# Optimization experiments

Measured on AMD Instinct MI355X. Metric: run time of the kernel, lower is better.

## Reference

```python
import jax, jax.numpy as jnp
import numpy as np
from jax import lax

B, T = 1024, 1000
EPS = 1e-3  # keras BatchNormalization default epsilon
ALPHA = 0.2  # tf.nn.leaky_relu default alpha


def setup_inputs() -> dict:
    key = jax.random.key(0)
    ks = jax.random.split(key, 40)
    f32 = jnp.float32
    n = lambda k, s, sc=0.1: jax.random.normal(k, s, dtype=f32) * sc
    inp = {"x": jax.random.normal(ks[0], (B, 2, T, 1), dtype=f32)}
    # main conv stack (HWIO kernels)
    inp["c1k"] = n(ks[1], (1, 5, 1, 10));  inp["c1b"] = n(ks[2], (10,), 0.01)
    inp["c2k"] = n(ks[3], (1, 5, 10, 10)); inp["c2b"] = n(ks[4], (10,), 0.01)
    inp["c3k"] = n(ks[5], (1, 5, 10, 10)); inp["c3b"] = n(ks[6], (10,), 0.01)
    inp["c4k"] = n(ks[7], (2, 1, 10, 20)); inp["c4b"] = n(ks[8], (20,), 0.01)
    # batchnorm (inference) params
    for i, k0 in zip((1, 2, 3), (9, 13, 17)):
        inp[f"g{i}"]  = 1.0 + n(ks[k0], (10,), 0.05)
        inp[f"be{i}"] = n(ks[k0 + 1], (10,), 0.05)
        inp[f"m{i}"]  = n(ks[k0 + 2], (10,), 0.05)
        inp[f"v{i}"]  = 1.0 + jax.random.uniform(ks[k0 + 3], (10,), dtype=f32) * 0.1
    # dense head: flatten of [B,1,T-12,20]
    inp["dns_w"] = n(ks[21], ((T - 12) * 20, 1), 0.02)
    inp["dns_b"] = jnp.zeros((1,), f32)
    # MHRSSA blocks: 10 heads of Conv2D(2,(2,1)) stacked -> K [10,2,Cin,2], b [10,2];
    # depthwise (1,5) over 10 channels -> dw [5,10], db [10]
    inp["a1K"] = n(ks[22], (10, 2, 1, 2));  inp["a1b"] = n(ks[23], (10, 2), 0.01)
    inp["a1dw"] = n(ks[24], (5, 10));       inp["a1db"] = n(ks[25], (10,), 0.01)
    inp["a2K"] = n(ks[26], (10, 2, 10, 2)); inp["a2b"] = n(ks[27], (10, 2), 0.01)
    inp["a2dw"] = n(ks[28], (5, 10));       inp["a2db"] = n(ks[29], (10,), 0.01)
    inp["a3K"] = n(ks[30], (10, 2, 10, 2)); inp["a3b"] = n(ks[31], (10, 2), 0.01)
    inp["a3dw"] = n(ks[32], (5, 10));       inp["a3db"] = n(ks[33], (10,), 0.01)
    return inp


def conv2d(x, k, b):
    return lax.conv_general_dilated(x, k, (1, 1), 'VALID',
                                    dimension_numbers=('NHWC', 'HWIO', 'NHWC')) + b


def bn_inf(x, g, be, m, v):
    return (x - m) * (g * lax.rsqrt(v + EPS)) + be


def lrelu(x):
    return jnp.where(x >= 0, x, ALPHA * x)


def mhrssa(x, K, b, dw, db):
    # x: [B,2,T,C]; K: [10,2,C,2] (10 heads of a (2,1)-valid conv) -> [B,10,T,2]
    m = jnp.einsum('bhtc,ihco->bito', x, K) + b[None, :, None, :]
    a = jnp.transpose(m, (0, 3, 2, 1))  # [B,2,T,10]
    Tt = a.shape[2]
    # depthwise (1,5) valid conv over time, per-channel taps dw[w,i]
    y = sum(a[:, :, w:w + Tt - 4, :] * dw[w] for w in range(5)) + db
    return jax.nn.softmax(y, axis=-1)


def reference(x, c1k, c1b, g1, be1, m1, v1, c2k, c2b, g2, be2, m2, v2,
              c3k, c3b, g3, be3, m3, v3, c4k, c4b, dns_w, dns_b,
              a1K, a1b, a1dw, a1db, a2K, a2b, a2dw, a2db, a3K, a3b, a3dw, a3db):
    att1 = mhrssa(x, a1K, a1b, a1dw, a1db)
    h = lrelu(bn_inf(conv2d(x, c1k, c1b), g1, be1, m1, v1)) * att1
    att2 = mhrssa(h, a2K, a2b, a2dw, a2db)
    h = lrelu(bn_inf(conv2d(h, c2k, c2b), g2, be2, m2, v2)) * att2
    att3 = mhrssa(h, a3K, a3b, a3dw, a3db)
    h = lrelu(bn_inf(conv2d(h, c3k, c3b), g3, be3, m3, v3)) * att3
    h = lrelu(conv2d(h, c4k, c4b))          # [B,1,T-12,20]
    h = h.reshape(h.shape[0], -1)
    return h @ dns_w + dns_b                # RGS mode: raw scalar output
```

## Files before the change

### kernel.cpp

```cpp
#include <hip/hip_runtime.h>

#define REP10(X) X(0) X(1) X(2) X(3) X(4) X(5) X(6) X(7) X(8) X(9)
#define REP5(X)  X(0) X(1) X(2) X(3) X(4)

typedef __attribute__((ext_vector_type(2))) float v2;

#define SMMP 136

__device__ __forceinline__ void fold_stage(
    float* dst, const float* g, const float* be, const float* mn,
    const float* vr, const float* cb, const float* adw, const float* adb,
    const float* aK, const float* ab, int CIN)
{
  const int tid = threadIdx.x;
  if (tid < 10) {
    const float sc = g[tid] * rsqrtf(vr[tid] + 1e-3f);
    dst[tid]      = sc;
    dst[10 + tid] = (cb[tid] - mn[tid]) * sc + be[tid];
    dst[70 + tid] = adb[tid] * 1.44269504088896340736f;
  }
  if (tid >= 10 && tid < 60)
    dst[10 + tid] = adw[tid - 10] * 1.44269504088896340736f;
  if (tid < 20)
    dst[80 + tid] = ab[(tid % 10) * 2 + tid / 10];
  const int n = 2 * CIN * 2 * 10;
  for (int idx = tid; idx < n; idx += 64) {
    const int i  = idx % 10;
    const int r  = idx / 10;
    const int o  = r % 2;
    const int r2 = r / 2;
    const int ci = r2 % CIN;
    const int h  = r2 / CIN;
    dst[100 + idx] = aK[((i * 2 + h) * CIN + ci) * 2 + o];
  }
}

__global__ void prep_kernel(
    const float* g1, const float* be1, const float* m1, const float* v1,
    const float* cb1, const float* a1dw, const float* a1db,
    const float* a1K, const float* a1b,
    const float* g2, const float* be2, const float* m2, const float* v2_,
    const float* cb2, const float* a2dw, const float* a2db,
    const float* a2K, const float* a2b,
    const float* g3, const float* be3, const float* m3, const float* v3,
    const float* cb3, const float* a3dw, const float* a3db,
    const float* a3K, const float* a3b,
    float* consts)
{
  fold_stage(consts,        g1, be1, m1, v1,  cb1, a1dw, a1db, a1K, a1b, 1);
  fold_stage(consts + 512,  g2, be2, m2, v2_, cb2, a2dw, a2db, a2K, a2b, 10);
  fold_stage(consts + 1024, g3, be3, m3, v3,  cb3, a3dw, a3db, a3K, a3b, 10);
}

__global__ void transpose_dnsw(const float* __restrict__ dnsw,
                               float* __restrict__ dnswT)
{
  const int cc = blockIdx.x;
  for (int t = threadIdx.x; t < 988; t += 256)
    dnswT[cc * 988 + t] = dnsw[t * 20 + cc];
}

template <int CIN>
__global__ __launch_bounds__(128) void stage_kernel(
    const float* __restrict__ in, float* __restrict__ outp, int Tout,
    const float* __restrict__ ck, const float* __restrict__ cst)
{
  __shared__ float smm[5 * SMMP * 2];
  const int tid = threadIdx.x;
  const int o   = blockIdx.y;
  const int t0  = blockIdx.x * 128;
  const int Tin = Tout + 4;
  const float* __restrict__ inb = in + (size_t)blockIdx.z * (CIN * 2000);

  const float* __restrict__ scale  = cst;
  const float* __restrict__ shift2 = cst + 10;
  const float* __restrict__ adw2   = cst + 20;
  const float* __restrict__ adb2   = cst + 70;
  const float* __restrict__ abp    = cst + 80;
  const float* __restrict__ aKp    = cst + 100;

  for (int lt = tid; lt < 132; lt += 128) {
    const int t = t0 + lt;
    if (t < Tin) {
#define DECLM(p) v2 mp##p = *reinterpret_cast<const v2*>(abp + o * 10 + 2 * p);
      REP5(DECLM)
#undef DECLM
#pragma unroll
      for (int h = 0; h < 2; ++h)
#pragma unroll
        for (int ci = 0; ci < CIN; ++ci) {
          const float xin = inb[(ci * 2 + h) * 1000 + t];
          const v2 xs = {xin, xin};
          const float* kb = aKp + ((h * CIN + ci) * 2 + o) * 10;
#define FMAM(p) mp##p = __builtin_elementwise_fma(                             \
              xs, *reinterpret_cast<const v2*>(kb + 2 * p), mp##p);
          REP5(FMAM)
#undef FMAM
        }
#define STM(p) *reinterpret_cast<v2*>(&smm[(p * SMMP + lt) * 2]) = mp##p;
      REP5(STM)
#undef STM
    }
  }
  __syncthreads();

  const int tt = t0 + tid;
  if (tt >= Tout) return;

#define DECLY(p) v2 yp##p = *reinterpret_cast<const v2*>(adb2 + 2 * p);
  REP5(DECLY)
#undef DECLY
#pragma unroll
  for (int w = 0; w < 5; ++w) {
    const float* aw = adw2 + w * 10;
#define FMAY(p) { const v2 sv =                                                \
        *reinterpret_cast<const v2*>(&smm[(p * SMMP + tid + w) * 2]);          \
      yp##p = __builtin_elementwise_fma(                                       \
          sv, *reinterpret_cast<const v2*>(aw + 2 * p), yp##p); }
    REP5(FMAY)
#undef FMAY
  }

#define DECLA(p) v2 ap##p = {0.f, 0.f};
  REP5(DECLA)
#undef DECLA
  const float* __restrict__ cinb = inb + o * 1000 + tt;
#pragma unroll
  for (int w = 0; w < 5; ++w)
#pragma unroll
    for (int ci = 0; ci < CIN; ++ci) {
      const float xin = cinb[ci * 2000 + w];
      const v2 xs = {xin, xin};
      const float* kb = ck + (w * CIN + ci) * 10;
#define FMAC(p) ap##p = __builtin_elementwise_fma(                             \
          xs, *reinterpret_cast<const v2*>(kb + 2 * p), ap##p);
      REP5(FMAC)
#undef FMAC
    }

  const float y0 = yp0.x, y1 = yp0.y, y2 = yp1.x, y3 = yp1.y, y4 = yp2.x,
              y5 = yp2.y, y6 = yp3.x, y7 = yp3.y, y8 = yp4.x, y9 = yp4.y;
  float mx = y0;
  mx = fmaxf(mx, y1); mx = fmaxf(mx, y2); mx = fmaxf(mx, y3);
  mx = fmaxf(mx, y4); mx = fmaxf(mx, y5); mx = fmaxf(mx, y6);
  mx = fmaxf(mx, y7); mx = fmaxf(mx, y8); mx = fmaxf(mx, y9);
#define DECLE(i) const float e##i = exp2f(y##i - mx);
  REP10(DECLE)
#undef DECLE
  const float sm  = e0 + e1 + e2 + e3 + e4 + e5 + e6 + e7 + e8 + e9;
  const float inv = __builtin_amdgcn_rcpf(sm);

  const float a0 = ap0.x, a1 = ap0.y, a2 = ap1.x, a3 = ap1.y, a4 = ap2.x,
              a5 = ap2.y, a6 = ap3.x, a7 = ap3.y, a8 = ap4.x, a9 = ap4.y;
  float* __restrict__ ob = outp + (size_t)blockIdx.z * 20000 + o * 1000 + tt;
#define STO(i) { float bv = a##i * scale[i] + shift2[i];                       \
    bv = fmaxf(bv, 0.2f * bv);                                                 \
    ob[i * 2000] = bv * e##i * inv; }
  REP10(STO)
#undef STO
}

__global__ __launch_bounds__(256) void final_kernel(
    const float* __restrict__ h3, const float* __restrict__ c4k,
    const float* __restrict__ c4b, const float* __restrict__ dnswT,
    const float* __restrict__ dnsb, float* __restrict__ outp, int b0)
{
  __shared__ float red[4];
  const int tid = threadIdx.x;
  const float* __restrict__ hb = h3 + (size_t)blockIdx.x * 20000;
  float partial = 0.f;
#pragma unroll 1
  for (int t = 2 * tid; t < 988; t += 512) {
#define LOADH(i)                                                               \
    const float2 xa##i = *reinterpret_cast<const float2*>(hb + i*2000 + t);    \
    const float2 xb##i = *reinterpret_cast<const float2*>(hb + i*2000 + 1000 + t);
    REP10(LOADH)
#undef LOADH
    float d0 = 0.f, d1 = 0.f;
#pragma unroll 4
    for (int cc = 0; cc < 20; ++cc) {
      const float bias = c4b[cc];
      float a0 = bias, a1 = bias;
#define FMA4(i) { const float wA = c4k[i*20 + cc], wB = c4k[(10+i)*20 + cc];   \
      a0 += xa##i.x * wA + xb##i.x * wB; a1 += xa##i.y * wA + xb##i.y * wB; }
      REP10(FMA4)
#undef FMA4
      a0 = fmaxf(a0, 0.2f * a0); a1 = fmaxf(a1, 0.2f * a1);
      const float2 dT = *reinterpret_cast<const float2*>(dnswT + cc * 988 + t);
      d0 += a0 * dT.x; d1 += a1 * dT.y;
    }
    partial += d0 + d1;
  }
#pragma unroll
  for (int off = 32; off > 0; off >>= 1)
    partial += __shfl_down(partial, off, 64);
  if ((tid & 63) == 0) red[tid >> 6] = partial;
  __syncthreads();
  if (tid == 0)
    outp[b0 + blockIdx.x] = red[0] + red[1] + red[2] + red[3] + dnsb[0];
}

extern "C" void kernel_launch(void* const* d_in, const int* in_sizes, int n_in,
                              void* d_out, int out_size, void* d_ws, size_t ws_size,
                              hipStream_t stream) {
  const float* p[35];
  for (int i = 0; i < 35; ++i) p[i] = (const float*)d_in[i];
  const int B = in_sizes[0] / 2000;

  float* consts = (float*)d_ws;
  float* dnswT  = consts + 1536;
  float* hA     = consts + 21296;
  const size_t avail = ws_size - 21296u * 4u;
  int CH = 1024;
  if (CH > B) CH = B;
  while ((size_t)CH * 160000ull > avail && CH > 1) CH >>= 1;
  float* hB = hA + (size_t)CH * 20000;

  prep_kernel<<<dim3(1), dim3(64), 0, stream>>>(
      p[9], p[10], p[11], p[12], p[2], p[25], p[26], p[23], p[24],
      p[13], p[14], p[15], p[16], p[4], p[29], p[30], p[27], p[28],
      p[17], p[18], p[19], p[20], p[6], p[33], p[34], p[31], p[32],
      consts);
  transpose_dnsw<<<dim3(20), dim3(256), 0, stream>>>(p[21], dnswT);

  for (int b0 = 0; b0 < B; b0 += CH) {
    const int cc = (B - b0 < CH) ? (B - b0) : CH;
    stage_kernel<1><<<dim3(8, 2, cc), dim3(128), 0, stream>>>(
        p[0] + (size_t)b0 * 2000, hA, 996, p[1], consts);
    stage_kernel<10><<<dim3(8, 2, cc), dim3(128), 0, stream>>>(
        hA, hB, 992, p[3], consts + 512);
    stage_kernel<10><<<dim3(8, 2, cc), dim3(128), 0, stream>>>(
        hB, hA, 988, p[5], consts + 1024);
    final_kernel<<<dim3(cc), dim3(256), 0, stream>>>(
        hA, p[7], p[8], dnswT, p[22], (float*)d_out, b0);
  }
}
```

Baseline: 175.1 us.

## Interleave channel pairs in intermediate activations for vectorized loads and stores

Intermediate activations are now stored as channel pairs interleaved along time ([pair][h][t][2]), so stage and final kernels read and write float2 vectors instead of scalar strided accesses. The final kernel is restructured to compute channel pairs with packed FMAs and read the dense weights in their original layout, which removes the separate transpose kernel and its workspace. The cost is more complex indexing and 8-byte strided accesses that may change coalescing behavior.

```diff
diff --git a/kernel.cpp b/kernel.cpp
--- a/kernel.cpp
+++ b/kernel.cpp
@@ -5,7 +5,7 @@
 
 typedef __attribute__((ext_vector_type(2))) float v2;
 
-#define SMMP 136
+#define SMX 136
 
 __device__ __forceinline__ void fold_stage(
     float* dst, const float* g, const float* be, const float* mn,
@@ -52,25 +52,18 @@
   fold_stage(consts + 1024, g3, be3, m3, v3,  cb3, a3dw, a3db, a3K, a3b, 10);
 }
 
-__global__ void transpose_dnsw(const float* __restrict__ dnsw,
-                               float* __restrict__ dnswT)
-{
-  const int cc = blockIdx.x;
-  for (int t = threadIdx.x; t < 988; t += 256)
-    dnswT[cc * 988 + t] = dnsw[t * 20 + cc];
-}
-
 template <int CIN>
 __global__ __launch_bounds__(128) void stage_kernel(
     const float* __restrict__ in, float* __restrict__ outp, int Tout,
     const float* __restrict__ ck, const float* __restrict__ cst)
 {
-  __shared__ float smm[5 * SMMP * 2];
+  __shared__ float smm[5 * SMX * 2];
   const int tid = threadIdx.x;
   const int o   = blockIdx.y;
   const int t0  = blockIdx.x * 128;
   const int Tin = Tout + 4;
-  const float* __restrict__ inb = in + (size_t)blockIdx.z * (CIN * 2000);
+  const float* __restrict__ inb =
+      in + (size_t)blockIdx.z * (CIN == 1 ? 2000 : 20000);
 
   const float* __restrict__ scale  = cst;
   const float* __restrict__ shift2 = cst + 10;
@@ -85,19 +78,37 @@
 #define DECLM(p) v2 mp##p = *reinterpret_cast<const v2*>(abp + o * 10 + 2 * p);
       REP5(DECLM)
 #undef DECLM
-#pragma unroll
-      for (int h = 0; h < 2; ++h)
-#pragma unroll
-        for (int ci = 0; ci < CIN; ++ci) {
-          const float xin = inb[(ci * 2 + h) * 1000 + t];
+      if constexpr (CIN == 1) {
+#pragma unroll
+        for (int h = 0; h < 2; ++h) {
+          const float xin = inb[h * 1000 + t];
           const v2 xs = {xin, xin};
-          const float* kb = aKp + ((h * CIN + ci) * 2 + o) * 10;
+          const float* kb = aKp + (h * 2 + o) * 10;
 #define FMAM(p) mp##p = __builtin_elementwise_fma(                             \
               xs, *reinterpret_cast<const v2*>(kb + 2 * p), mp##p);
           REP5(FMAM)
 #undef FMAM
         }
-#define STM(p) *reinterpret_cast<v2*>(&smm[(p * SMMP + lt) * 2]) = mp##p;
+      } else {
+#pragma unroll
+        for (int h = 0; h < 2; ++h)
+#pragma unroll
+          for (int pc = 0; pc < 5; ++pc) {
+            const v2 xv = *reinterpret_cast<const v2*>(
+                inb + ((pc * 2 + h) * 1000 + t) * 2);
+            const v2 xs0 = {xv.x, xv.x};
+            const v2 xs1 = {xv.y, xv.y};
+            const float* kb0 = aKp + ((h * CIN + 2 * pc) * 2 + o) * 10;
+            const float* kb1 = aKp + ((h * CIN + 2 * pc + 1) * 2 + o) * 10;
+#define FMAM(p) mp##p = __builtin_elementwise_fma(                             \
+                xs0, *reinterpret_cast<const v2*>(kb0 + 2 * p), mp##p);        \
+            mp##p = __builtin_elementwise_fma(                                 \
+                xs1, *reinterpret_cast<const v2*>(kb1 + 2 * p), mp##p);
+            REP5(FMAM)
+#undef FMAM
+          }
+      }
+#define STM(p) *reinterpret_cast<v2*>(&smm[(p * SMX + lt) * 2]) = mp##p;
       REP5(STM)
 #undef STM
     }
@@ -114,7 +125,7 @@
   for (int w = 0; w < 5; ++w) {
     const float* aw = adw2 + w * 10;
 #define FMAY(p) { const v2 sv =                                                \
-        *reinterpret_cast<const v2*>(&smm[(p * SMMP + tid + w) * 2]);          \
+        *reinterpret_cast<const v2*>(&smm[(p * SMX + tid + w) * 2]);           \
       yp##p = __builtin_elementwise_fma(                                       \
           sv, *reinterpret_cast<const v2*>(aw + 2 * p), yp##p); }
     REP5(FMAY)
@@ -124,19 +135,37 @@
 #define DECLA(p) v2 ap##p = {0.f, 0.f};
   REP5(DECLA)
 #undef DECLA
-  const float* __restrict__ cinb = inb + o * 1000 + tt;
-#pragma unroll
-  for (int w = 0; w < 5; ++w)
-#pragma unroll
-    for (int ci = 0; ci < CIN; ++ci) {
-      const float xin = cinb[ci * 2000 + w];
+  if constexpr (CIN == 1) {
+    const float* __restrict__ cinb = inb + o * 1000 + tt;
+#pragma unroll
+    for (int w = 0; w < 5; ++w) {
+      const float xin = cinb[w];
       const v2 xs = {xin, xin};
-      const float* kb = ck + (w * CIN + ci) * 10;
+      const float* kb = ck + w * 10;
 #define FMAC(p) ap##p = __builtin_elementwise_fma(                             \
           xs, *reinterpret_cast<const v2*>(kb + 2 * p), ap##p);
       REP5(FMAC)
 #undef FMAC
     }
+  } else {
+#pragma unroll
+    for (int w = 0; w < 5; ++w)
+#pragma unroll
+      for (int pc = 0; pc < 5; ++pc) {
+        const v2 xv = *reinterpret_cast<const v2*>(
+            inb + ((pc * 2 + o) * 1000 + tt + w) * 2);
+        const v2 xs0 = {xv.x, xv.x};
+        const v2 xs1 = {xv.y, xv.y};
+        const float* kb0 = ck + (w * CIN + 2 * pc) * 10;
+        const float* kb1 = ck + (w * CIN + 2 * pc + 1) * 10;
+#define FMAC(p) ap##p = __builtin_elementwise_fma(                             \
+            xs0, *reinterpret_cast<const v2*>(kb0 + 2 * p), ap##p);            \
+        ap##p = __builtin_elementwise_fma(                                     \
+            xs1, *reinterpret_cast<const v2*>(kb1 + 2 * p), ap##p);
+        REP5(FMAC)
+#undef FMAC
+      }
+  }
 
   const float y0 = yp0.x, y1 = yp0.y, y2 = yp1.x, y3 = yp1.y, y4 = yp2.x,
               y5 = yp2.y, y6 = yp3.x, y7 = yp3.y, y8 = yp4.x, y9 = yp4.y;
@@ -150,47 +179,59 @@
   const float sm  = e0 + e1 + e2 + e3 + e4 + e5 + e6 + e7 + e8 + e9;
   const float inv = __builtin_amdgcn_rcpf(sm);
 
-  const float a0 = ap0.x, a1 = ap0.y, a2 = ap1.x, a3 = ap1.y, a4 = ap2.x,
-              a5 = ap2.y, a6 = ap3.x, a7 = ap3.y, a8 = ap4.x, a9 = ap4.y;
-  float* __restrict__ ob = outp + (size_t)blockIdx.z * 20000 + o * 1000 + tt;
-#define STO(i) { float bv = a##i * scale[i] + shift2[i];                       \
-    bv = fmaxf(bv, 0.2f * bv);                                                 \
-    ob[i * 2000] = bv * e##i * inv; }
-  REP10(STO)
+  float* __restrict__ ob =
+      outp + (size_t)blockIdx.z * 20000 + (o * 1000 + tt) * 2;
+#define STO(p, ea, eb) {                                                       \
+    v2 bv = __builtin_elementwise_fma(                                         \
+        ap##p, *reinterpret_cast<const v2*>(scale + 2 * p),                    \
+        *reinterpret_cast<const v2*>(shift2 + 2 * p));                         \
+    bv = __builtin_elementwise_max(bv, 0.2f * bv);                             \
+    const v2 ev = {ea * inv, eb * inv};                                        \
+    *reinterpret_cast<v2*>(ob + p * 4000) = bv * ev; }
+  STO(0, e0, e1) STO(1, e2, e3) STO(2, e4, e5) STO(3, e6, e7) STO(4, e8, e9)
 #undef STO
 }
 
 __global__ __launch_bounds__(256) void final_kernel(
     const float* __restrict__ h3, const float* __restrict__ c4k,
-    const float* __restrict__ c4b, const float* __restrict__ dnswT,
+    const float* __restrict__ c4b, const float* __restrict__ dnsw,
     const float* __restrict__ dnsb, float* __restrict__ outp, int b0)
 {
   __shared__ float red[4];
   const int tid = threadIdx.x;
   const float* __restrict__ hb = h3 + (size_t)blockIdx.x * 20000;
-  float partial = 0.f;
+  v2 dotv = {0.f, 0.f};
 #pragma unroll 1
-  for (int t = 2 * tid; t < 988; t += 512) {
-#define LOADH(i)                                                               \
-    const float2 xa##i = *reinterpret_cast<const float2*>(hb + i*2000 + t);    \
-    const float2 xb##i = *reinterpret_cast<const float2*>(hb + i*2000 + 1000 + t);
-    REP10(LOADH)
-#undef LOADH
-    float d0 = 0.f, d1 = 0.f;
-#pragma unroll 4
-    for (int cc = 0; cc < 20; ++cc) {
-      const float bias = c4b[cc];
-      float a0 = bias, a1 = bias;
-#define FMA4(i) { const float wA = c4k[i*20 + cc], wB = c4k[(10+i)*20 + cc];   \
-      a0 += xa##i.x * wA + xb##i.x * wB; a1 += xa##i.y * wA + xb##i.y * wB; }
-      REP10(FMA4)
+  for (int t = tid; t < 988; t += 256) {
+#define LDX(p)                                                                 \
+    const v2 xa##p = *reinterpret_cast<const v2*>(hb + ((p*2+0)*1000 + t)*2);  \
+    const v2 xc##p = *reinterpret_cast<const v2*>(hb + ((p*2+1)*1000 + t)*2);
+    REP5(LDX)
+#undef LDX
+    const float* __restrict__ dwp = dnsw + t * 20;
+#pragma unroll
+    for (int q = 0; q < 10; ++q) {
+      v2 acc = *reinterpret_cast<const v2*>(c4b + 2 * q);
+      const float* kq = c4k + 2 * q;
+#define FMA4(p) {                                                              \
+      const v2 s0 = {xa##p.x, xa##p.x}, s1 = {xa##p.y, xa##p.y};               \
+      const v2 s2 = {xc##p.x, xc##p.x}, s3 = {xc##p.y, xc##p.y};               \
+      acc = __builtin_elementwise_fma(                                         \
+          s0, *reinterpret_cast<const v2*>(kq + (2*p) * 20), acc);             \
+      acc = __builtin_elementwise_fma(                                         \
+          s1, *reinterpret_cast<const v2*>(kq + (2*p+1) * 20), acc);           \
+      acc = __builtin_elementwise_fma(                                         \
+          s2, *reinterpret_cast<const v2*>(kq + (10+2*p) * 20), acc);          \
+      acc = __builtin_elementwise_fma(                                         \
+          s3, *reinterpret_cast<const v2*>(kq + (10+2*p+1) * 20), acc); }
+      REP5(FMA4)
 #undef FMA4
-      a0 = fmaxf(a0, 0.2f * a0); a1 = fmaxf(a1, 0.2f * a1);
-      const float2 dT = *reinterpret_cast<const float2*>(dnswT + cc * 988 + t);
-      d0 += a0 * dT.x; d1 += a1 * dT.y;
+      acc  = __builtin_elementwise_max(acc, 0.2f * acc);
+      dotv = __builtin_elementwise_fma(
+          acc, *reinterpret_cast<const v2*>(dwp + 2 * q), dotv);
     }
-    partial += d0 + d1;
-  }
+  }
+  float partial = dotv.x + dotv.y;
 #pragma unroll
   for (int off = 32; off > 0; off >>= 1)
     partial += __shfl_down(partial, off, 64);
@@ -208,9 +249,8 @@
   const int B = in_sizes[0] / 2000;
 
   float* consts = (float*)d_ws;
-  float* dnswT  = consts + 1536;
-  float* hA     = consts + 21296;
-  const size_t avail = ws_size - 21296u * 4u;
+  float* hA     = consts + 1536;
+  const size_t avail = ws_size - 1536u * 4u;
   int CH = 1024;
   if (CH > B) CH = B;
   while ((size_t)CH * 160000ull > avail && CH > 1) CH >>= 1;
@@ -221,7 +261,6 @@
       p[13], p[14], p[15], p[16], p[4], p[29], p[30], p[27], p[28],
       p[17], p[18], p[19], p[20], p[6], p[33], p[34], p[31], p[32],
       consts);
-  transpose_dnsw<<<dim3(20), dim3(256), 0, stream>>>(p[21], dnswT);
 
   for (int b0 = 0; b0 < B; b0 += CH) {
     const int cc = (B - b0 < CH) ? (B - b0) : CH;
@@ -232,6 +271,6 @@
     stage_kernel<10><<<dim3(8, 2, cc), dim3(128), 0, stream>>>(
         hB, hA, 988, p[5], consts + 1024);
     final_kernel<<<dim3(cc), dim3(256), 0, stream>>>(
-        hA, p[7], p[8], dnswT, p[22], (float*)d_out, b0);
-  }
-}
+        hA, p[7], p[8], p[21], p[22], (float*)d_out, b0);
+  }
+}
```

Result: no change. 172.8 us (-1.3%).
